# Optimization experiments

Measured on AMD Instinct MI355X. Metric: run time of the kernel, lower is better.

## Reference

```python
import jax, jax.numpy as jnp
import numpy as np

GRID = 10
C_IN = 4          # input_dim // (grid*grid) = 400 // 100
HID = 128         # lstm hidden_dim
NV = 6            # num_vehicles
PH = 10           # pred_horizon
BN_EPS = 1e-5


def setup_inputs() -> dict:
    key = jax.random.key(0)
    ks = jax.random.split(key, 20)
    def n(k, shape, scale=0.05):
        return jax.random.normal(k, shape, jnp.float32) * scale
    return {
        "observations": jax.random.normal(ks[0], (1024, 32, 400), jnp.float32),
        # CNN
        "conv1_w": n(ks[1], (16, C_IN, 3, 3)), "conv1_b": n(ks[2], (16,)),
        "conv2_w": n(ks[3], (32, 16, 3, 3)), "conv2_b": n(ks[4], (32,)),
        # FCN (BatchNorm in eval mode: running stats + affine)
        "fc1_w": n(ks[5], (128, 128)), "fc1_b": n(ks[6], (128,)),
        "bn1_gamma": jnp.ones((128,), jnp.float32), "bn1_beta": jnp.zeros((128,), jnp.float32),
        "bn1_mean": jnp.zeros((128,), jnp.float32), "bn1_var": jnp.ones((128,), jnp.float32),
        "fc2_w": n(ks[7], (64, 128)), "fc2_b": n(ks[8], (64,)),
        "bn2_gamma": jnp.ones((64,), jnp.float32), "bn2_beta": jnp.zeros((64,), jnp.float32),
        "bn2_mean": jnp.zeros((64,), jnp.float32), "bn2_var": jnp.ones((64,), jnp.float32),
        # encoder LSTM (torch gate order i,f,g,o; b = b_ih + b_hh fused)
        "enc_w_ih": n(ks[9], (4 * HID, 64)), "enc_w_hh": n(ks[10], (4 * HID, HID)),
        "enc_b": n(ks[11], (4 * HID,)),
        # decoder LSTM
        "dec_w_ih": n(ks[12], (4 * HID, HID)), "dec_w_hh": n(ks[13], (4 * HID, HID)),
        "dec_b": n(ks[14], (4 * HID,)),
        # output head
        "out_w": n(ks[15], (2 * NV, HID)), "out_b": n(ks[16], (2 * NV,)),
    }


def _conv(x, w, b):
    y = jax.lax.conv_general_dilated(x, w, (1, 1), "SAME",
                                     dimension_numbers=("NCHW", "OIHW", "NCHW"))
    return y + b[None, :, None, None]


def _maxpool2(x):
    # MaxPool2d(2,2) with floor (drops odd trailing row/col) == VALID
    return jax.lax.reduce_window(x, -jnp.inf, jax.lax.max, (1, 1, 2, 2), (1, 1, 2, 2), "VALID")


def _bn(x, g, b, m, v):
    return (x - m) * jax.lax.rsqrt(v + BN_EPS) * g + b


def _lstm_cell(x, h, c, w_ih, w_hh, b):
    gates = x @ w_ih.T + h @ w_hh.T + b
    i, f, g, o = jnp.split(gates, 4, axis=-1)
    c_new = jax.nn.sigmoid(f) * c + jax.nn.sigmoid(i) * jnp.tanh(g)
    h_new = jax.nn.sigmoid(o) * jnp.tanh(c_new)
    return h_new, c_new


def reference(observations, conv1_w, conv1_b, conv2_w, conv2_b,
              fc1_w, fc1_b, bn1_gamma, bn1_beta, bn1_mean, bn1_var,
              fc2_w, fc2_b, bn2_gamma, bn2_beta, bn2_mean, bn2_var,
              enc_w_ih, enc_w_hh, enc_b, dec_w_ih, dec_w_hh, dec_b,
              out_w, out_b):
    B, T, D = observations.shape
    # ---- fuse the per-frame Python loop: batch all B*T frames at once ----
    x = observations.reshape(B * T, C_IN, GRID, GRID)
    x = _maxpool2(jax.nn.relu(_conv(x, conv1_w, conv1_b)))   # [BT,16,5,5]
    x = _maxpool2(jax.nn.relu(_conv(x, conv2_w, conv2_b)))   # [BT,32,2,2]
    x = x.reshape(B * T, -1)                                 # [BT,128]
    x = jax.nn.relu(_bn(x @ fc1_w.T + fc1_b, bn1_gamma, bn1_beta, bn1_mean, bn1_var))
    x = jax.nn.relu(_bn(x @ fc2_w.T + fc2_b, bn2_gamma, bn2_beta, bn2_mean, bn2_var))
    feats = x.reshape(B, T, 64)

    # ---- encoder LSTM ----
    h0 = jnp.zeros((B, HID), feats.dtype)
    c0 = jnp.zeros((B, HID), feats.dtype)
    def enc_step(carry, xt):
        h, c = carry
        h, c = _lstm_cell(xt, h, c, enc_w_ih, enc_w_hh, enc_b)
        return (h, c), h
    (h_n, c_n), hs = jax.lax.scan(enc_step, (h0, c0), jnp.swapaxes(feats, 0, 1))
    dec_x = hs[-1]  # encoder_output[:, -1]

    def dec_step(carry, _):
        x_in, h, c = carry
        h, c = _lstm_cell(x_in, h, c, dec_w_ih, dec_w_hh, dec_b)
        pred = h @ out_w.T + out_b
        return (h, h, c), pred
    _, preds = jax.lax.scan(dec_step, (dec_x, h_n, c_n), None, length=PH)
    return jnp.swapaxes(preds, 0, 1)  # [B, PH, 2*NV]
```

## Files before the change

kernel.cpp:

```cpp
#include <hip/hip_runtime.h>
#include <hip/hip_bf16.h>
#include <hip/hip_fp16.h>

constexpr int GT = 32768;
constexpr int TSEQ = 32;

typedef _Float16 h2 __attribute__((ext_vector_type(2)));

#if defined(__has_builtin)
#if __has_builtin(__builtin_amdgcn_fdot2)
#define FDOT2(a, b, c) __builtin_amdgcn_fdot2((a), (b), (c), false)
#endif
#endif
#ifndef FDOT2
#define FDOT2(a, b, c) fmaf((float)(a).x, (float)(b).x, fmaf((float)(a).y, (float)(b).y, (c)))
#endif

__device__ __forceinline__ h2 pack2(float a, float b) {
  h2 v; v.x = (_Float16)a; v.y = (_Float16)b; return v;
}

constexpr size_t OBS_T  = 0;
constexpr size_t POOL1H = 13107200;
constexpr size_t POOL2H = 0;
constexpr size_t Y1H    = 2097152;
constexpr size_t FEATSH = 19660800;
constexpr size_t GX     = 0;
constexpr size_t WB     = 26214400;
constexpr size_t W_C1   = WB + 0;
constexpr size_t W_C2H  = WB + 576;
constexpr size_t W_F1H  = WB + 2880;
constexpr size_t B_F1   = WB + 11072;
constexpr size_t W_F2H  = WB + 11200;
constexpr size_t B_F2   = WB + 15296;
constexpr size_t W_ENCXH= WB + 15360;
constexpr size_t W_ENCHH= WB + 31744;
constexpr size_t B_ENC  = WB + 64512;
constexpr size_t W_DECH = WB + 65024;
constexpr size_t B_DEC  = WB + 97792;

__device__ __forceinline__ float sigf(float x)  { return 1.f / (1.f + __expf(-x)); }
__device__ __forceinline__ float tanhfast(float x) { return 1.f - 2.f / (__expf(2.f * x) + 1.f); }

__global__ __launch_bounds__(256) void k_setup(
    const float* __restrict__ c1w, const float* __restrict__ c2w,
    const float* __restrict__ f1w, const float* __restrict__ f1b,
    const float* __restrict__ g1, const float* __restrict__ be1,
    const float* __restrict__ m1, const float* __restrict__ v1,
    const float* __restrict__ f2w, const float* __restrict__ f2b,
    const float* __restrict__ g2, const float* __restrict__ be2,
    const float* __restrict__ m2, const float* __restrict__ v2,
    const float* __restrict__ ewih, const float* __restrict__ ewhh, const float* __restrict__ eb,
    const float* __restrict__ dwih, const float* __restrict__ dwhh, const float* __restrict__ db,
    float* __restrict__ ws) {
  h2* wsh = (h2*)ws;
  long i = (long)blockIdx.x * 256 + threadIdx.x;
  if (i < 576)  { int c = i & 15, r = i >> 4; ws[W_C1 + i] = c1w[c * 36 + r]; return; }
  i -= 576;
  if (i < 2304) { int co = i & 31, q = i >> 5; int ci2 = q / 9, t9 = q % 9;
    wsh[W_C2H + i] = pack2(c2w[co * 144 + (2 * ci2) * 9 + t9],
                           c2w[co * 144 + (2 * ci2 + 1) * 9 + t9]); return; }
  i -= 2304;
  if (i < 8192) { int j = i & 127, q = i >> 7; int co2 = q >> 2, pos = q & 3;
    float s = g1[j] * rsqrtf(v1[j] + 1e-5f);
    wsh[W_F1H + i] = pack2(f1w[j * 128 + 8 * co2 + pos] * s,
                           f1w[j * 128 + 8 * co2 + 4 + pos] * s); return; }
  i -= 8192;
  if (i < 128) { int j = i; float s = g1[j] * rsqrtf(v1[j] + 1e-5f);
    ws[B_F1 + i] = (f1b[j] - m1[j]) * s + be1[j]; return; }
  i -= 128;
  if (i < 4096) { int j = i & 63, k2 = i >> 6;
    float s = g2[j] * rsqrtf(v2[j] + 1e-5f);
    wsh[W_F2H + i] = pack2(f2w[j * 128 + 2 * k2] * s,
                           f2w[j * 128 + 2 * k2 + 1] * s); return; }
  i -= 4096;
  if (i < 64) { int j = i; float s = g2[j] * rsqrtf(v2[j] + 1e-5f);
    ws[B_F2 + i] = (f2b[j] - m2[j]) * s + be2[j]; return; }
  i -= 64;
  if (i < 16384) { int r = i & 511, k2 = i >> 9;
    int u = r >> 2, gt = r & 3, jr = gt * 128 + u;
    wsh[W_ENCXH + i] = pack2(ewih[jr * 64 + 2 * k2], ewih[jr * 64 + 2 * k2 + 1]); return; }
  i -= 16384;
  if (i < 32768) { int r = i & 511, k2 = i >> 9;
    int u = r >> 2, gt = r & 3, jr = gt * 128 + u;
    wsh[W_ENCHH + i] = pack2(ewhh[jr * 128 + 2 * k2], ewhh[jr * 128 + 2 * k2 + 1]); return; }
  i -= 32768;
  if (i < 512) { int u = i >> 2, gt = i & 3; ws[B_ENC + i] = eb[gt * 128 + u]; return; }
  i -= 512;
  if (i < 32768) { int r = i & 511, k2 = i >> 9;
    int u = r >> 2, gt = r & 3, jr = gt * 128 + u;
    wsh[W_DECH + i] = pack2(dwih[jr * 128 + 2 * k2] + dwhh[jr * 128 + 2 * k2],
                            dwih[jr * 128 + 2 * k2 + 1] + dwhh[jr * 128 + 2 * k2 + 1]); return; }
  i -= 32768;
  if (i < 512) { int u = i >> 2, gt = i & 3; ws[B_DEC + i] = db[gt * 128 + u]; return; }
}

__global__ __launch_bounds__(256) void k_transpose(const float* __restrict__ obs,
                                                   float* __restrict__ obsT) {
  __shared__ float tile[64][65];
  int tp0 = blockIdx.x * 64;
  int b0  = blockIdx.y * 64;
  int q     = threadIdx.x & 15;
  int rbase = threadIdx.x >> 4;
  #pragma unroll
  for (int rr = 0; rr < 4; ++rr) {
    int row = rbase + rr * 16;
    const float4 v = *(const float4*)(obs + (size_t)(b0 + row) * 12800 + tp0 + q * 4);
    tile[row][q * 4 + 0] = v.x;
    tile[row][q * 4 + 1] = v.y;
    tile[row][q * 4 + 2] = v.z;
    tile[row][q * 4 + 3] = v.w;
  }
  __syncthreads();
  int lane = threadIdx.x & 63;
  int grp  = threadIdx.x >> 6;
  for (int cc = 0; cc < 16; ++cc) {
    int col = grp * 16 + cc;
    int tp = tp0 + col;
    int t = tp / 400, p = tp % 400;
    obsT[(size_t)p * GT + t * 1024 + b0 + lane] = tile[lane][col];
  }
}

__global__ __launch_bounds__(256) void k_conv1(const float* __restrict__ obsT,
                                               const float* __restrict__ wT,
                                               const float* __restrict__ bias,
                                               h2* __restrict__ pool1h) {
  int g = blockIdx.x * 256 + threadIdx.x;
  int pos = blockIdx.y;
  int py = pos / 5, px = pos % 5;
  float acc[4][16];
  #pragma unroll
  for (int s = 0; s < 4; ++s)
    #pragma unroll
    for (int c = 0; c < 16; ++c) acc[s][c] = 0.f;

  #pragma unroll 1
  for (int ci = 0; ci < 4; ++ci) {
    float p[16];
    #pragma unroll
    for (int r = 0; r < 4; ++r) {
      int iy = 2 * py + r - 1;
      #pragma unroll
      for (int cx = 0; cx < 4; ++cx) {
        int ix = 2 * px + cx - 1;
        bool ok = ((unsigned)iy < 10u) && ((unsigned)ix < 10u);
        p[r * 4 + cx] = ok ? obsT[(size_t)(ci * 100 + iy * 10 + ix) * GT + g] : 0.f;
      }
    }
    #pragma unroll
    for (int t9 = 0; t9 < 9; ++t9) {
      int ky = t9 / 3, kx = t9 % 3;
      const float* w = wT + ((ci * 9 + t9) << 4);
      float wv[16];
      #pragma unroll
      for (int c = 0; c < 16; ++c) wv[c] = w[c];
      #pragma unroll
      for (int dy = 0; dy < 2; ++dy)
        #pragma unroll
        for (int dx = 0; dx < 2; ++dx) {
          float xv = p[(dy + ky) * 4 + (dx + kx)];
          #pragma unroll
          for (int c = 0; c < 16; ++c)
            acc[dy * 2 + dx][c] = fmaf(wv[c], xv, acc[dy * 2 + dx][c]);
        }
    }
  }
  float m[16];
  #pragma unroll
  for (int c = 0; c < 16; ++c) {
    float v = fmaxf(fmaxf(acc[0][c], acc[1][c]), fmaxf(acc[2][c], acc[3][c]));
    m[c] = fmaxf(v + bias[c], 0.f);
  }
  #pragma unroll
  for (int c2 = 0; c2 < 8; ++c2)
    pool1h[(size_t)(c2 * 25 + pos) * GT + g] = pack2(m[2 * c2], m[2 * c2 + 1]);
}

__global__ __launch_bounds__(256) void k_conv2h(const h2* __restrict__ pool1h,
                                                const h2* __restrict__ wch,
                                                const float* __restrict__ bias,
                                                h2* __restrict__ pool2h) {
  int g = blockIdx.x * 256 + threadIdx.x;
  int pos = blockIdx.y & 3;
  int h = blockIdx.y >> 2;
  int py = pos >> 1, px = pos & 1;
  float acc[4][8];
  #pragma unroll
  for (int s = 0; s < 4; ++s)
    #pragma unroll
    for (int c = 0; c < 8; ++c) acc[s][c] = 0.f;
  const h2 hz = pack2(0.f, 0.f);

  #pragma unroll 1
  for (int ci2 = 0; ci2 < 8; ++ci2) {
    h2 p[16];
    #pragma unroll
    for (int r = 0; r < 4; ++r) {
      int iy = 2 * py + r - 1;
      #pragma unroll
      for (int cx = 0; cx < 4; ++cx) {
        int ix = 2 * px + cx - 1;
        bool ok = ((unsigned)iy < 5u) && ((unsigned)ix < 5u);
        p[r * 4 + cx] = ok ? pool1h[(size_t)(ci2 * 25 + iy * 5 + ix) * GT + g] : hz;
      }
    }
    #pragma unroll
    for (int t9 = 0; t9 < 9; ++t9) {
      int ky = t9 / 3, kx = t9 % 3;
      const h2* w = wch + (ci2 * 9 + t9) * 32 + h * 8;
      h2 wv[8];
      #pragma unroll
      for (int c = 0; c < 8; ++c) wv[c] = w[c];
      #pragma unroll
      for (int dy = 0; dy < 2; ++dy)
        #pragma unroll
        for (int dx = 0; dx < 2; ++dx) {
          h2 xv = p[(dy + ky) * 4 + (dx + kx)];
          #pragma unroll
          for (int c = 0; c < 8; ++c)
            acc[dy * 2 + dx][c] = FDOT2(xv, wv[c], acc[dy * 2 + dx][c]);
        }
    }
  }
  float m[8];
  #pragma unroll
  for (int c = 0; c < 8; ++c) {
    float v = fmaxf(fmaxf(acc[0][c], acc[1][c]), fmaxf(acc[2][c], acc[3][c]));
    m[c] = fmaxf(v + bias[h * 8 + c], 0.f);
  }
  #pragma unroll
  for (int c2 = 0; c2 < 4; ++c2) {
    int q = (h * 4 + c2) * 4 + pos;
    pool2h[(size_t)q * GT + g] = pack2(m[2 * c2], m[2 * c2 + 1]);
  }
}

__global__ __launch_bounds__(256) void k_fc16h(const h2* __restrict__ x,
                                               const h2* __restrict__ WT,
                                               const float* __restrict__ bf,
                                               h2* __restrict__ y, int K2, int J) {
  int g = blockIdx.x * 256 + threadIdx.x;
  int j0 = blockIdx.y * 16;
  float acc[16];
  #pragma unroll
  for (int c = 0; c < 16; ++c) acc[c] = 0.f;
  for (int k2 = 0; k2 < K2; ++k2) {
    h2 xv = x[(size_t)k2 * GT + g];
    const h2* w = WT + (size_t)k2 * J + j0;
    #pragma unroll
    for (int c = 0; c < 16; ++c) acc[c] = FDOT2(xv, w[c], acc[c]);
  }
  #pragma unroll
  for (int c2 = 0; c2 < 8; ++c2) {
    float a = fmaxf(acc[2 * c2] + bf[j0 + 2 * c2], 0.f);
    float b = fmaxf(acc[2 * c2 + 1] + bf[j0 + 2 * c2 + 1], 0.f);
    y[(size_t)(j0 / 2 + c2) * GT + g] = pack2(a, b);
  }
}

__global__ __launch_bounds__(256) void k_xgatesh(const h2* __restrict__ featsh,
                                                 const h2* __restrict__ wxh,
                                                 const float* __restrict__ br,
                                                 float* __restrict__ gx) {
  int t  = blockIdx.x >> 2;
  int bq = blockIdx.x & 3;
  int b  = bq * 256 + threadIdx.x;
  int r0 = blockIdx.y * 32;
  float acc[32];
  #pragma unroll
  for (int i = 0; i < 32; ++i) acc[i] = br[r0 + i];
  const h2* xcol = featsh + (size_t)t * 1024 + b;
  for (int k2 = 0; k2 < 32; ++k2) {
    h2 xv = xcol[(size_t)k2 * GT];
    const h2* w = wxh + k2 * 512 + r0;
    #pragma unroll
    for (int i = 0; i < 32; ++i) acc[i] = FDOT2(xv, w[i], acc[i]);
  }
  float* gxs = gx + (size_t)t * 524288 + (size_t)b * 512 + r0;
  #pragma unroll
  for (int i = 0; i < 32; ++i) gxs[i] = acc[i];
}

__global__ __launch_bounds__(512, 2) void k_seq6(
    const float* __restrict__ gx,
    const h2* __restrict__ WENCH, const h2* __restrict__ WDECH,
    const float* __restrict__ bdec,
    const float* __restrict__ ow, const float* __restrict__ ob,
    float* __restrict__ out) {
  const int tid = threadIdx.x;
  const int kg  = tid & 7;
  const int g   = tid >> 3;
  const int r0  = g * 8;
  const int blo = kg & 3;
  const int bown = blockIdx.x * 4 + blo;

  __shared__ h2 hbufh[2][4 * 68];
  __shared__ h2 owl2[12 * 68];

  for (int i = tid; i < 2 * 4 * 68; i += 512) hbufh[0][i] = pack2(0.f, 0.f);
  for (int i = tid; i < 768; i += 512) {
    int o = i >> 6, k2 = i & 63;
    owl2[o * 68 + k2] = pack2(ow[o * 128 + 2 * k2], ow[o * 128 + 2 * k2 + 1]);
  }
  const float obv = (tid < 48) ? ob[tid >> 2] : 0.f;

  h2 wreg[64];
  #pragma unroll
  for (int p = 0; p < 8; ++p) {
    const h2* wp = WENCH + (size_t)(kg * 8 + p) * 512 + r0;
    *(uint4*)&wreg[p * 8]     = *(const uint4*)wp;
    *(uint4*)&wreg[p * 8 + 4] = *(const uint4*)(wp + 4);
  }

  float c0 = 0.f, c1 = 0.f;
  const int rdofs = kg * 8;
  const int wrofs = blo * 68 + g;
  __syncthreads();

  int cur = 0;

  for (int t = 0; t < TSEQ; ++t) {
    const float* gb0 = gx + (size_t)t * 524288 + (size_t)bown * 512 + r0;
    const float4 ga = *(const float4*)gb0;
    const float4 gb = *(const float4*)(gb0 + 4);

    float acc[4][8];
    #pragma unroll
    for (int bl = 0; bl < 4; ++bl)
      #pragma unroll
      for (int r = 0; r < 8; ++r) acc[bl][r] = 0.f;

    const h2* hc = &hbufh[cur][0];
    #pragma unroll
    for (int bl = 0; bl < 4; ++bl) {
      h2 hv[8];
      *(uint4*)&hv[0] = *(const uint4*)&hc[bl * 68 + rdofs];
      *(uint4*)&hv[4] = *(const uint4*)&hc[bl * 68 + rdofs + 4];
      #pragma unroll
      for (int p = 0; p < 8; ++p) {
        #pragma unroll
        for (int r = 0; r < 8; ++r)
          acc[bl][r] = FDOT2(hv[p], wreg[p * 8 + r], acc[bl][r]);
      }
    }
    float D[8];
    #pragma unroll
    for (int r = 0; r < 8; ++r) {
      float a0 = acc[0][r] + __shfl_xor(acc[0][r], 1, 64);
      float a1 = acc[1][r] + __shfl_xor(acc[1][r], 1, 64);
      float a2 = acc[2][r] + __shfl_xor(acc[2][r], 1, 64);
      float a3 = acc[3][r] + __shfl_xor(acc[3][r], 1, 64);
      float sL = (kg & 1) ? a1 : a0;
      float sH = (kg & 1) ? a3 : a2;
      float tL = sL + __shfl_xor(sL, 2, 64);
      float tH = sH + __shfl_xor(sH, 2, 64);
      float s  = (kg & 2) ? tH : tL;
      s += __shfl_xor(s, 4, 64);
      D[r] = s;
    }
    const float gi0 = D[0] + ga.x, gf0 = D[1] + ga.y, gg0 = D[2] + ga.z, go0 = D[3] + ga.w;
    const float gi1 = D[4] + gb.x, gf1 = D[5] + gb.y, gg1 = D[6] + gb.z, go1 = D[7] + gb.w;
    c0 = sigf(gf0) * c0 + sigf(gi0) * tanhfast(gg0);
    c1 = sigf(gf1) * c1 + sigf(gi1) * tanhfast(gg1);
    const float hn0 = sigf(go0) * tanhfast(c0);
    const float hn1 = sigf(go1) * tanhfast(c1);
    if (kg < 4) hbufh[cur ^ 1][wrofs] = pack2(hn0, hn1);
    __syncthreads();
    cur ^= 1;
  }

  #pragma unroll
  for (int p = 0; p < 8; ++p) {
    const h2* wp = WDECH + (size_t)(kg * 8 + p) * 512 + r0;
    *(uint4*)&wreg[p * 8]     = *(const uint4*)wp;
    *(uint4*)&wreg[p * 8 + 4] = *(const uint4*)(wp + 4);
  }
  const float4 bda = *(const float4*)(bdec + r0);
  const float4 bdb = *(const float4*)(bdec + r0 + 4);

  for (int t = 0; t < 10; ++t) {
    float acc[4][8];
    #pragma unroll
    for (int bl = 0; bl < 4; ++bl)
      #pragma unroll
      for (int r = 0; r < 8; ++r) acc[bl][r] = 0.f;

    const h2* hc = &hbufh[cur][0];
    #pragma unroll
    for (int bl = 0; bl < 4; ++bl) {
      h2 hv[8];
      *(uint4*)&hv[0] = *(const uint4*)&hc[bl * 68 + rdofs];
      *(uint4*)&hv[4] = *(const uint4*)&hc[bl * 68 + rdofs + 4];
      #pragma unroll
      for (int p = 0; p < 8; ++p) {
        #pragma unroll
        for (int r = 0; r < 8; ++r)
          acc[bl][r] = FDOT2(hv[p], wreg[p * 8 + r], acc[bl][r]);
      }
    }
    float D[8];
    #pragma unroll
    for (int r = 0; r < 8; ++r) {
      float a0 = acc[0][r] + __shfl_xor(acc[0][r], 1, 64);
      float a1 = acc[1][r] + __shfl_xor(acc[1][r], 1, 64);
      float a2 = acc[2][r] + __shfl_xor(acc[2][r], 1, 64);
      float a3 = acc[3][r] + __shfl_xor(acc[3][r], 1, 64);
      float sL = (kg & 1) ? a1 : a0;
      float sH = (kg & 1) ? a3 : a2;
      float tL = sL + __shfl_xor(sL, 2, 64);
      float tH = sH + __shfl_xor(sH, 2, 64);
      float s  = (kg & 2) ? tH : tL;
      s += __shfl_xor(s, 4, 64);
      D[r] = s;
    }
    const float gi0 = D[0] + bda.x, gf0 = D[1] + bda.y, gg0 = D[2] + bda.z, go0 = D[3] + bda.w;
    const float gi1 = D[4] + bdb.x, gf1 = D[5] + bdb.y, gg1 = D[6] + bdb.z, go1 = D[7] + bdb.w;
    c0 = sigf(gf0) * c0 + sigf(gi0) * tanhfast(gg0);
    c1 = sigf(gf1) * c1 + sigf(gi1) * tanhfast(gg1);
    const float hn0 = sigf(go0) * tanhfast(c0);
    const float hn1 = sigf(go1) * tanhfast(c1);
    if (kg < 4) hbufh[cur ^ 1][wrofs] = pack2(hn0, hn1);
    __syncthreads();
    cur ^= 1;
    if (tid < 48) {
      const int o  = tid >> 2;
      const int bh = tid & 3;
      const h2* hh = &hbufh[cur][bh * 68];
      const h2* wo = &owl2[o * 68];
      float oacc = obv;
      #pragma unroll
      for (int k2 = 0; k2 < 64; ++k2) oacc = FDOT2(hh[k2], wo[k2], oacc);
      out[(blockIdx.x * 4 + bh) * 120 + t * 12 + o] = oacc;
    }
  }
}

extern "C" void kernel_launch(void* const* d_in, const int* in_sizes, int n_in,
                              void* d_out, int out_size, void* d_ws, size_t ws_size,
                              hipStream_t stream) {
  const float* obs  = (const float*)d_in[0];
  const float* c1w  = (const float*)d_in[1];
  const float* c1b  = (const float*)d_in[2];
  const float* c2w  = (const float*)d_in[3];
  const float* c2b  = (const float*)d_in[4];
  const float* f1w  = (const float*)d_in[5];
  const float* f1b  = (const float*)d_in[6];
  const float* g1   = (const float*)d_in[7];
  const float* be1  = (const float*)d_in[8];
  const float* m1   = (const float*)d_in[9];
  const float* v1   = (const float*)d_in[10];
  const float* f2w  = (const float*)d_in[11];
  const float* f2b  = (const float*)d_in[12];
  const float* g2   = (const float*)d_in[13];
  const float* be2  = (const float*)d_in[14];
  const float* m2   = (const float*)d_in[15];
  const float* v2   = (const float*)d_in[16];
  const float* ewih = (const float*)d_in[17];
  const float* ewhh = (const float*)d_in[18];
  const float* eb   = (const float*)d_in[19];
  const float* dwih = (const float*)d_in[20];
  const float* dwhh = (const float*)d_in[21];
  const float* db   = (const float*)d_in[22];
  const float* ow   = (const float*)d_in[23];
  const float* ob   = (const float*)d_in[24];
  float* ws  = (float*)d_ws;
  h2*    wsh = (h2*)d_ws;
  float* out = (float*)d_out;

  k_setup<<<384, 256, 0, stream>>>(c1w, c2w, f1w, f1b, g1, be1, m1, v1,
                                   f2w, f2b, g2, be2, m2, v2,
                                   ewih, ewhh, eb, dwih, dwhh, db, ws);
  k_transpose<<<dim3(200, 16), 256, 0, stream>>>(obs, ws + OBS_T);
  k_conv1<<<dim3(128, 25), 256, 0, stream>>>(ws + OBS_T, ws + W_C1, c1b, wsh + POOL1H);
  k_conv2h<<<dim3(128, 16), 256, 0, stream>>>(wsh + POOL1H, wsh + W_C2H, c2b, wsh + POOL2H);
  k_fc16h<<<dim3(128, 8), 256, 0, stream>>>(wsh + POOL2H, wsh + W_F1H, ws + B_F1,
                                            wsh + Y1H, 64, 128);
  k_fc16h<<<dim3(128, 4), 256, 0, stream>>>(wsh + Y1H, wsh + W_F2H, ws + B_F2,
                                            wsh + FEATSH, 64, 64);
  k_xgatesh<<<dim3(128, 16), 256, 0, stream>>>(wsh + FEATSH, wsh + W_ENCXH, ws + B_ENC,
                                               ws + GX);
  k_seq6<<<256, 512, 0, stream>>>(ws + GX, wsh + W_ENCHH, wsh + W_DECH,
                                  ws + B_DEC, ow, ob, out);
}
```

Before: 408.7 us.

## Pack observations to fp16 in transpose, fp16 conv1, wider tiles, halve LSTM batch per block

The transpose kernel now packs channel pairs into fp16 halves, and conv1 uses fdot2 on the packed input, which halves the transposed-observation traffic. Conv2, the FC layers and the x-gate kernel each compute twice as many outputs per thread, so input reloads drop. The recurrent LSTM kernel now handles 2 batch rows per block over 512 blocks instead of 4 rows over 256, which spreads the sequential work across more CUs. The costs are higher register pressure from the wider accumulators and extra fp16 rounding on the conv1 input.

New measurement: 479.8 us. +17.4%, slower.

```diff
diff --git a/kernel.cpp b/kernel.cpp
--- a/kernel.cpp
+++ b/kernel.cpp
@@ -20,24 +20,24 @@
   h2 v; v.x = (_Float16)a; v.y = (_Float16)b; return v;
 }
 
-constexpr size_t OBS_T  = 0;
-constexpr size_t POOL1H = 13107200;
+constexpr size_t OBS_TH = 0;
+constexpr size_t POOL1H = 6553600;
 constexpr size_t POOL2H = 0;
 constexpr size_t Y1H    = 2097152;
-constexpr size_t FEATSH = 19660800;
-constexpr size_t GX     = 0;
+constexpr size_t FEATSH = 4194304;
+constexpr size_t GX     = 6553600;
 constexpr size_t WB     = 26214400;
-constexpr size_t W_C1   = WB + 0;
-constexpr size_t W_C2H  = WB + 576;
-constexpr size_t W_F1H  = WB + 2880;
-constexpr size_t B_F1   = WB + 11072;
-constexpr size_t W_F2H  = WB + 11200;
-constexpr size_t B_F2   = WB + 15296;
-constexpr size_t W_ENCXH= WB + 15360;
-constexpr size_t W_ENCHH= WB + 31744;
-constexpr size_t B_ENC  = WB + 64512;
-constexpr size_t W_DECH = WB + 65024;
-constexpr size_t B_DEC  = WB + 97792;
+constexpr size_t W_C1H  = WB + 0;
+constexpr size_t W_C2H  = WB + 288;
+constexpr size_t W_F1H  = WB + 2592;
+constexpr size_t B_F1   = WB + 10784;
+constexpr size_t W_F2H  = WB + 10912;
+constexpr size_t B_F2   = WB + 15008;
+constexpr size_t W_ENCXH= WB + 15072;
+constexpr size_t W_ENCHH= WB + 31456;
+constexpr size_t B_ENC  = WB + 64224;
+constexpr size_t W_DECH = WB + 64736;
+constexpr size_t B_DEC  = WB + 97504;
 
 __device__ __forceinline__ float sigf(float x)  { return 1.f / (1.f + __expf(-x)); }
 __device__ __forceinline__ float tanhfast(float x) { return 1.f - 2.f / (__expf(2.f * x) + 1.f); }
@@ -55,8 +55,10 @@
     float* __restrict__ ws) {
   h2* wsh = (h2*)ws;
   long i = (long)blockIdx.x * 256 + threadIdx.x;
-  if (i < 576)  { int c = i & 15, r = i >> 4; ws[W_C1 + i] = c1w[c * 36 + r]; return; }
-  i -= 576;
+  if (i < 288) { int co = i & 15, q = i >> 4; int ci2 = q / 9, t9 = q % 9;
+    wsh[W_C1H + i] = pack2(c1w[co * 36 + 2 * ci2 * 9 + t9],
+                           c1w[co * 36 + (2 * ci2 + 1) * 9 + t9]); return; }
+  i -= 288;
   if (i < 2304) { int co = i & 31, q = i >> 5; int ci2 = q / 9, t9 = q % 9;
     wsh[W_C2H + i] = pack2(c2w[co * 144 + (2 * ci2) * 9 + t9],
                            c2w[co * 144 + (2 * ci2 + 1) * 9 + t9]); return; }
@@ -95,37 +97,37 @@
   if (i < 512) { int u = i >> 2, gt = i & 3; ws[B_DEC + i] = db[gt * 128 + u]; return; }
 }
 
-__global__ __launch_bounds__(256) void k_transpose(const float* __restrict__ obs,
-                                                   float* __restrict__ obsT) {
-  __shared__ float tile[64][65];
-  int tp0 = blockIdx.x * 64;
-  int b0  = blockIdx.y * 64;
-  int q     = threadIdx.x & 15;
-  int rbase = threadIdx.x >> 4;
-  #pragma unroll
-  for (int rr = 0; rr < 4; ++rr) {
-    int row = rbase + rr * 16;
-    const float4 v = *(const float4*)(obs + (size_t)(b0 + row) * 12800 + tp0 + q * 4);
-    tile[row][q * 4 + 0] = v.x;
-    tile[row][q * 4 + 1] = v.y;
-    tile[row][q * 4 + 2] = v.z;
-    tile[row][q * 4 + 3] = v.w;
-  }
-  __syncthreads();
-  int lane = threadIdx.x & 63;
-  int grp  = threadIdx.x >> 6;
-  for (int cc = 0; cc < 16; ++cc) {
-    int col = grp * 16 + cc;
-    int tp = tp0 + col;
-    int t = tp / 400, p = tp % 400;
-    obsT[(size_t)p * GT + t * 1024 + b0 + lane] = tile[lane][col];
-  }
-}
-
-__global__ __launch_bounds__(256) void k_conv1(const float* __restrict__ obsT,
-                                               const float* __restrict__ wT,
-                                               const float* __restrict__ bias,
-                                               h2* __restrict__ pool1h) {
+__global__ __launch_bounds__(256) void k_transpose_pack(const float* __restrict__ obs,
+                                                        h2* __restrict__ obsTh) {
+  __shared__ float sm[2][4][4][64];
+  const int pix0 = blockIdx.x * 4;
+  const int b0   = blockIdx.y * 64;
+  const int lane = threadIdx.x & 63;
+  const int grp  = threadIdx.x >> 6;
+  const int ci2  = grp >> 1;
+  const int q0   = (grp & 1) * 2;
+  for (int t = 0; t < 32; ++t) {
+    const int buf = t & 1;
+    const float4 v = *(const float4*)(obs + (size_t)(b0 + lane) * 12800
+                                      + t * 400 + grp * 100 + pix0);
+    sm[buf][grp][0][lane] = v.x;
+    sm[buf][grp][1][lane] = v.y;
+    sm[buf][grp][2][lane] = v.z;
+    sm[buf][grp][3][lane] = v.w;
+    __syncthreads();
+    #pragma unroll
+    for (int qq = 0; qq < 2; ++qq) {
+      const int q = q0 + qq;
+      h2 val = pack2(sm[buf][2 * ci2][q][lane], sm[buf][2 * ci2 + 1][q][lane]);
+      obsTh[(size_t)(ci2 * 100 + pix0 + q) * GT + t * 1024 + b0 + lane] = val;
+    }
+  }
+}
+
+__global__ __launch_bounds__(256) void k_conv1h(const h2* __restrict__ obsTh,
+                                                const h2* __restrict__ wch,
+                                                const float* __restrict__ bias,
+                                                h2* __restrict__ pool1h) {
   int g = blockIdx.x * 256 + threadIdx.x;
   int pos = blockIdx.y;
   int py = pos / 5, px = pos % 5;
@@ -134,10 +136,11 @@
   for (int s = 0; s < 4; ++s)
     #pragma unroll
     for (int c = 0; c < 16; ++c) acc[s][c] = 0.f;
-
-  #pragma unroll 1
-  for (int ci = 0; ci < 4; ++ci) {
-    float p[16];
+  const h2 hz = pack2(0.f, 0.f);
+
+  #pragma unroll
+  for (int ci2 = 0; ci2 < 2; ++ci2) {
+    h2 p[16];
     #pragma unroll
     for (int r = 0; r < 4; ++r) {
       int iy = 2 * py + r - 1;
@@ -145,24 +148,24 @@
       for (int cx = 0; cx < 4; ++cx) {
         int ix = 2 * px + cx - 1;
         bool ok = ((unsigned)iy < 10u) && ((unsigned)ix < 10u);
-        p[r * 4 + cx] = ok ? obsT[(size_t)(ci * 100 + iy * 10 + ix) * GT + g] : 0.f;
+        p[r * 4 + cx] = ok ? obsTh[(size_t)(ci2 * 100 + iy * 10 + ix) * GT + g] : hz;
       }
     }
     #pragma unroll
     for (int t9 = 0; t9 < 9; ++t9) {
       int ky = t9 / 3, kx = t9 % 3;
-      const float* w = wT + ((ci * 9 + t9) << 4);
-      float wv[16];
+      const h2* w = wch + ((ci2 * 9 + t9) << 4);
+      h2 wv[16];
       #pragma unroll
       for (int c = 0; c < 16; ++c) wv[c] = w[c];
       #pragma unroll
       for (int dy = 0; dy < 2; ++dy)
         #pragma unroll
         for (int dx = 0; dx < 2; ++dx) {
-          float xv = p[(dy + ky) * 4 + (dx + kx)];
+          h2 xv = p[(dy + ky) * 4 + (dx + kx)];
           #pragma unroll
           for (int c = 0; c < 16; ++c)
-            acc[dy * 2 + dx][c] = fmaf(wv[c], xv, acc[dy * 2 + dx][c]);
+            acc[dy * 2 + dx][c] = FDOT2(xv, wv[c], acc[dy * 2 + dx][c]);
         }
     }
   }
@@ -185,11 +188,11 @@
   int pos = blockIdx.y & 3;
   int h = blockIdx.y >> 2;
   int py = pos >> 1, px = pos & 1;
-  float acc[4][8];
+  float acc[4][16];
   #pragma unroll
   for (int s = 0; s < 4; ++s)
     #pragma unroll
-    for (int c = 0; c < 8; ++c) acc[s][c] = 0.f;
+    for (int c = 0; c < 16; ++c) acc[s][c] = 0.f;
   const h2 hz = pack2(0.f, 0.f);
 
   #pragma unroll 1
@@ -208,51 +211,51 @@
     #pragma unroll
     for (int t9 = 0; t9 < 9; ++t9) {
       int ky = t9 / 3, kx = t9 % 3;
-      const h2* w = wch + (ci2 * 9 + t9) * 32 + h * 8;
-      h2 wv[8];
-      #pragma unroll
-      for (int c = 0; c < 8; ++c) wv[c] = w[c];
+      const h2* w = wch + (ci2 * 9 + t9) * 32 + h * 16;
+      h2 wv[16];
+      #pragma unroll
+      for (int c = 0; c < 16; ++c) wv[c] = w[c];
       #pragma unroll
       for (int dy = 0; dy < 2; ++dy)
         #pragma unroll
         for (int dx = 0; dx < 2; ++dx) {
           h2 xv = p[(dy + ky) * 4 + (dx + kx)];
           #pragma unroll
-          for (int c = 0; c < 8; ++c)
+          for (int c = 0; c < 16; ++c)
             acc[dy * 2 + dx][c] = FDOT2(xv, wv[c], acc[dy * 2 + dx][c]);
         }
     }
   }
-  float m[8];
-  #pragma unroll
-  for (int c = 0; c < 8; ++c) {
+  float m[16];
+  #pragma unroll
+  for (int c = 0; c < 16; ++c) {
     float v = fmaxf(fmaxf(acc[0][c], acc[1][c]), fmaxf(acc[2][c], acc[3][c]));
-    m[c] = fmaxf(v + bias[h * 8 + c], 0.f);
-  }
-  #pragma unroll
-  for (int c2 = 0; c2 < 4; ++c2) {
-    int q = (h * 4 + c2) * 4 + pos;
+    m[c] = fmaxf(v + bias[h * 16 + c], 0.f);
+  }
+  #pragma unroll
+  for (int c2 = 0; c2 < 8; ++c2) {
+    int q = (h * 8 + c2) * 4 + pos;
     pool2h[(size_t)q * GT + g] = pack2(m[2 * c2], m[2 * c2 + 1]);
   }
 }
 
-__global__ __launch_bounds__(256) void k_fc16h(const h2* __restrict__ x,
+__global__ __launch_bounds__(256) void k_fc32h(const h2* __restrict__ x,
                                                const h2* __restrict__ WT,
                                                const float* __restrict__ bf,
                                                h2* __restrict__ y, int K2, int J) {
   int g = blockIdx.x * 256 + threadIdx.x;
-  int j0 = blockIdx.y * 16;
-  float acc[16];
-  #pragma unroll
-  for (int c = 0; c < 16; ++c) acc[c] = 0.f;
+  int j0 = blockIdx.y * 32;
+  float acc[32];
+  #pragma unroll
+  for (int c = 0; c < 32; ++c) acc[c] = 0.f;
   for (int k2 = 0; k2 < K2; ++k2) {
     h2 xv = x[(size_t)k2 * GT + g];
     const h2* w = WT + (size_t)k2 * J + j0;
     #pragma unroll
-    for (int c = 0; c < 16; ++c) acc[c] = FDOT2(xv, w[c], acc[c]);
-  }
-  #pragma unroll
-  for (int c2 = 0; c2 < 8; ++c2) {
+    for (int c = 0; c < 32; ++c) acc[c] = FDOT2(xv, w[c], acc[c]);
+  }
+  #pragma unroll
+  for (int c2 = 0; c2 < 16; ++c2) {
     float a = fmaxf(acc[2 * c2] + bf[j0 + 2 * c2], 0.f);
     float b = fmaxf(acc[2 * c2 + 1] + bf[j0 + 2 * c2 + 1], 0.f);
     y[(size_t)(j0 / 2 + c2) * GT + g] = pack2(a, b);
@@ -266,23 +269,23 @@
   int t  = blockIdx.x >> 2;
   int bq = blockIdx.x & 3;
   int b  = bq * 256 + threadIdx.x;
-  int r0 = blockIdx.y * 32;
-  float acc[32];
-  #pragma unroll
-  for (int i = 0; i < 32; ++i) acc[i] = br[r0 + i];
+  int r0 = blockIdx.y * 64;
+  float acc[64];
+  #pragma unroll
+  for (int i = 0; i < 64; ++i) acc[i] = br[r0 + i];
   const h2* xcol = featsh + (size_t)t * 1024 + b;
   for (int k2 = 0; k2 < 32; ++k2) {
     h2 xv = xcol[(size_t)k2 * GT];
     const h2* w = wxh + k2 * 512 + r0;
     #pragma unroll
-    for (int i = 0; i < 32; ++i) acc[i] = FDOT2(xv, w[i], acc[i]);
+    for (int i = 0; i < 64; ++i) acc[i] = FDOT2(xv, w[i], acc[i]);
   }
   float* gxs = gx + (size_t)t * 524288 + (size_t)b * 512 + r0;
   #pragma unroll
-  for (int i = 0; i < 32; ++i) gxs[i] = acc[i];
-}
-
-__global__ __launch_bounds__(512, 2) void k_seq6(
+  for (int i = 0; i < 64; ++i) gxs[i] = acc[i];
+}
+
+__global__ __launch_bounds__(512, 2) void k_seq7(
     const float* __restrict__ gx,
     const h2* __restrict__ WENCH, const h2* __restrict__ WDECH,
     const float* __restrict__ bdec,
@@ -292,18 +295,18 @@
   const int kg  = tid & 7;
   const int g   = tid >> 3;
   const int r0  = g * 8;
-  const int blo = kg & 3;
-  const int bown = blockIdx.x * 4 + blo;
-
-  __shared__ h2 hbufh[2][4 * 68];
+  const int blo = kg & 1;
+  const int bown = blockIdx.x * 2 + blo;
+
+  __shared__ h2 hbufh[2][2 * 68];
   __shared__ h2 owl2[12 * 68];
 
-  for (int i = tid; i < 2 * 4 * 68; i += 512) hbufh[0][i] = pack2(0.f, 0.f);
+  for (int i = tid; i < 2 * 2 * 68; i += 512) ((h2*)hbufh)[i] = pack2(0.f, 0.f);
   for (int i = tid; i < 768; i += 512) {
     int o = i >> 6, k2 = i & 63;
     owl2[o * 68 + k2] = pack2(ow[o * 128 + 2 * k2], ow[o * 128 + 2 * k2 + 1]);
   }
-  const float obv = (tid < 48) ? ob[tid >> 2] : 0.f;
+  const float obv = (tid < 24) ? ob[tid >> 1] : 0.f;
 
   h2 wreg[64];
   #pragma unroll
@@ -325,23 +328,24 @@
     const float4 ga = *(const float4*)gb0;
     const float4 gb = *(const float4*)(gb0 + 4);
 
-    float acc[4][8];
-    #pragma unroll
-    for (int bl = 0; bl < 4; ++bl)
+    float acc[2][8];
+    #pragma unroll
+    for (int bl = 0; bl < 2; ++bl)
       #pragma unroll
       for (int r = 0; r < 8; ++r) acc[bl][r] = 0.f;
 
     const h2* hc = &hbufh[cur][0];
-    #pragma unroll
-    for (int bl = 0; bl < 4; ++bl) {
-      h2 hv[8];
-      *(uint4*)&hv[0] = *(const uint4*)&hc[bl * 68 + rdofs];
-      *(uint4*)&hv[4] = *(const uint4*)&hc[bl * 68 + rdofs + 4];
-      #pragma unroll
-      for (int p = 0; p < 8; ++p) {
-        #pragma unroll
-        for (int r = 0; r < 8; ++r)
-          acc[bl][r] = FDOT2(hv[p], wreg[p * 8 + r], acc[bl][r]);
+    h2 hv0[8], hv1[8];
+    *(uint4*)&hv0[0] = *(const uint4*)&hc[rdofs];
+    *(uint4*)&hv0[4] = *(const uint4*)&hc[rdofs + 4];
+    *(uint4*)&hv1[0] = *(const uint4*)&hc[68 + rdofs];
+    *(uint4*)&hv1[4] = *(const uint4*)&hc[68 + rdofs + 4];
+    #pragma unroll
+    for (int p = 0; p < 8; ++p) {
+      #pragma unroll
+      for (int r = 0; r < 8; ++r) {
+        acc[0][r] = FDOT2(hv0[p], wreg[p * 8 + r], acc[0][r]);
+        acc[1][r] = FDOT2(hv1[p], wreg[p * 8 + r], acc[1][r]);
       }
     }
     float D[8];
@@ -349,13 +353,8 @@
     for (int r = 0; r < 8; ++r) {
       float a0 = acc[0][r] + __shfl_xor(acc[0][r], 1, 64);
       float a1 = acc[1][r] + __shfl_xor(acc[1][r], 1, 64);
-      float a2 = acc[2][r] + __shfl_xor(acc[2][r], 1, 64);
-      float a3 = acc[3][r] + __shfl_xor(acc[3][r], 1, 64);
-      float sL = (kg & 1) ? a1 : a0;
-      float sH = (kg & 1) ? a3 : a2;
-      float tL = sL + __shfl_xor(sL, 2, 64);
-      float tH = sH + __shfl_xor(sH, 2, 64);
-      float s  = (kg & 2) ? tH : tL;
+      float s  = blo ? a1 : a0;
+      s += __shfl_xor(s, 2, 64);
       s += __shfl_xor(s, 4, 64);
       D[r] = s;
     }
@@ -365,7 +364,7 @@
     c1 = sigf(gf1) * c1 + sigf(gi1) * tanhfast(gg1);
     const float hn0 = sigf(go0) * tanhfast(c0);
     const float hn1 = sigf(go1) * tanhfast(c1);
-    if (kg < 4) hbufh[cur ^ 1][wrofs] = pack2(hn0, hn1);
+    if (kg < 2) hbufh[cur ^ 1][wrofs] = pack2(hn0, hn1);
     __syncthreads();
     cur ^= 1;
   }
@@ -380,23 +379,24 @@
   const float4 bdb = *(const float4*)(bdec + r0 + 4);
 
   for (int t = 0; t < 10; ++t) {
-    float acc[4][8];
-    #pragma unroll
-    for (int bl = 0; bl < 4; ++bl)
+    float acc[2][8];
+    #pragma unroll
+    for (int bl = 0; bl < 2; ++bl)
       #pragma unroll
       for (int r = 0; r < 8; ++r) acc[bl][r] = 0.f;
 
     const h2* hc = &hbufh[cur][0];
-    #pragma unroll
-    for (int bl = 0; bl < 4; ++bl) {
-      h2 hv[8];
-      *(uint4*)&hv[0] = *(const uint4*)&hc[bl * 68 + rdofs];
-      *(uint4*)&hv[4] = *(const uint4*)&hc[bl * 68 + rdofs + 4];
-      #pragma unroll
-      for (int p = 0; p < 8; ++p) {
-        #pragma unroll
-        for (int r = 0; r < 8; ++r)
-          acc[bl][r] = FDOT2(hv[p], wreg[p * 8 + r], acc[bl][r]);
+    h2 hv0[8], hv1[8];
+    *(uint4*)&hv0[0] = *(const uint4*)&hc[rdofs];
+    *(uint4*)&hv0[4] = *(const uint4*)&hc[rdofs + 4];
+    *(uint4*)&hv1[0] = *(const uint4*)&hc[68 + rdofs];
+    *(uint4*)&hv1[4] = *(const uint4*)&hc[68 + rdofs + 4];
+    #pragma unroll
+    for (int p = 0; p < 8; ++p) {
+      #pragma unroll
+      for (int r = 0; r < 8; ++r) {
+        acc[0][r] = FDOT2(hv0[p], wreg[p * 8 + r], acc[0][r]);
+        acc[1][r] = FDOT2(hv1[p], wreg[p * 8 + r], acc[1][r]);
       }
     }
     float D[8];
@@ -404,13 +404,8 @@
     for (int r = 0; r < 8; ++r) {
       float a0 = acc[0][r] + __shfl_xor(acc[0][r], 1, 64);
       float a1 = acc[1][r] + __shfl_xor(acc[1][r], 1, 64);
-      float a2 = acc[2][r] + __shfl_xor(acc[2][r], 1, 64);
-      float a3 = acc[3][r] + __shfl_xor(acc[3][r], 1, 64);
-      float sL = (kg & 1) ? a1 : a0;
-      float sH = (kg & 1) ? a3 : a2;
-      float tL = sL + __shfl_xor(sL, 2, 64);
-      float tH = sH + __shfl_xor(sH, 2, 64);
-      float s  = (kg & 2) ? tH : tL;
+      float s  = blo ? a1 : a0;
+      s += __shfl_xor(s, 2, 64);
       s += __shfl_xor(s, 4, 64);
       D[r] = s;
     }
@@ -420,18 +415,18 @@
     c1 = sigf(gf1) * c1 + sigf(gi1) * tanhfast(gg1);
     const float hn0 = sigf(go0) * tanhfast(c0);
     const float hn1 = sigf(go1) * tanhfast(c1);
-    if (kg < 4) hbufh[cur ^ 1][wrofs] = pack2(hn0, hn1);
+    if (kg < 2) hbufh[cur ^ 1][wrofs] = pack2(hn0, hn1);
     __syncthreads();
     cur ^= 1;
-    if (tid < 48) {
-      const int o  = tid >> 2;
-      const int bh = tid & 3;
+    if (tid < 24) {
+      const int o  = tid >> 1;
+      const int bh = tid & 1;
       const h2* hh = &hbufh[cur][bh * 68];
       const h2* wo = &owl2[o * 68];
       float oacc = obv;
       #pragma unroll
       for (int k2 = 0; k2 < 64; ++k2) oacc = FDOT2(hh[k2], wo[k2], oacc);
-      out[(blockIdx.x * 4 + bh) * 120 + t * 12 + o] = oacc;
+      out[(blockIdx.x * 2 + bh) * 120 + t * 12 + o] = oacc;
     }
   }
 }
@@ -468,18 +463,18 @@
   h2*    wsh = (h2*)d_ws;
   float* out = (float*)d_out;
 
-  k_setup<<<384, 256, 0, stream>>>(c1w, c2w, f1w, f1b, g1, be1, m1, v1,
+  k_setup<<<383, 256, 0, stream>>>(c1w, c2w, f1w, f1b, g1, be1, m1, v1,
                                    f2w, f2b, g2, be2, m2, v2,
                                    ewih, ewhh, eb, dwih, dwhh, db, ws);
-  k_transpose<<<dim3(200, 16), 256, 0, stream>>>(obs, ws + OBS_T);
-  k_conv1<<<dim3(128, 25), 256, 0, stream>>>(ws + OBS_T, ws + W_C1, c1b, wsh + POOL1H);
-  k_conv2h<<<dim3(128, 16), 256, 0, stream>>>(wsh + POOL1H, wsh + W_C2H, c2b, wsh + POOL2H);
-  k_fc16h<<<dim3(128, 8), 256, 0, stream>>>(wsh + POOL2H, wsh + W_F1H, ws + B_F1,
+  k_transpose_pack<<<dim3(25, 16), 256, 0, stream>>>(obs, wsh + OBS_TH);
+  k_conv1h<<<dim3(128, 25), 256, 0, stream>>>(wsh + OBS_TH, wsh + W_C1H, c1b, wsh + POOL1H);
+  k_conv2h<<<dim3(128, 8), 256, 0, stream>>>(wsh + POOL1H, wsh + W_C2H, c2b, wsh + POOL2H);
+  k_fc32h<<<dim3(128, 4), 256, 0, stream>>>(wsh + POOL2H, wsh + W_F1H, ws + B_F1,
                                             wsh + Y1H, 64, 128);
-  k_fc16h<<<dim3(128, 4), 256, 0, stream>>>(wsh + Y1H, wsh + W_F2H, ws + B_F2,
+  k_fc32h<<<dim3(128, 2), 256, 0, stream>>>(wsh + Y1H, wsh + W_F2H, ws + B_F2,
                                             wsh + FEATSH, 64, 64);
-  k_xgatesh<<<dim3(128, 16), 256, 0, stream>>>(wsh + FEATSH, wsh + W_ENCXH, ws + B_ENC,
-                                               ws + GX);
-  k_seq6<<<256, 512, 0, stream>>>(ws + GX, wsh + W_ENCHH, wsh + W_DECH,
+  k_xgatesh<<<dim3(128, 8), 256, 0, stream>>>(wsh + FEATSH, wsh + W_ENCXH, ws + B_ENC,
+                                              ws + GX);
+  k_seq7<<<512, 512, 0, stream>>>(ws + GX, wsh + W_ENCHH, wsh + W_DECH,
                                   ws + B_DEC, ow, ob, out);
 }
```
